# Performance work log

Measured on AMD Instinct MI355X. Metric: run time of the kernel, lower is better.

## Reference

```python
import jax, jax.numpy as jnp
import numpy as np

NUM_PPR_NODES = 262144
BATCH = 4096
K = NUM_PPR_NODES // BATCH  # ppr neighbors per batch node
F_IN, H, C = 256, 512, 64


def setup_inputs() -> dict:
    key = jax.random.key(0)
    ks = jax.random.split(key, 6)
    X = jax.random.normal(ks[0], (NUM_PPR_NODES, F_IN), dtype=jnp.float32)
    ppr_scores = jax.random.uniform(ks[1], (NUM_PPR_NODES,), dtype=jnp.float32)
    # sorted batch ids; last element == BATCH-1 so dim_size = ppr_idx[-1]+1 = BATCH
    ppr_idx = jnp.repeat(jnp.arange(BATCH, dtype=jnp.int64), K)
    s1 = 1.0 / np.sqrt(F_IN)
    s2 = 1.0 / np.sqrt(H)
    Wa = jax.random.uniform(ks[2], (F_IN, H), jnp.float32, -s1, s1)
    Wb = jax.random.uniform(ks[3], (H, H), jnp.float32, -s2, s2)
    Wc = jax.random.uniform(ks[4], (H, H), jnp.float32, -s2, s2)
    Wd = jax.random.uniform(ks[5], (H, C), jnp.float32, -s2, s2)
    return {"X": X, "ppr_scores": ppr_scores, "ppr_idx": ppr_idx,
            "Wa": Wa, "Wb": Wb, "Wc": Wc, "Wd": Wd}


def reference(X, ppr_scores, ppr_idx, Wa, Wb, Wc, Wd):
    # embedding MLP (dropout inactive at eval): Linear -> ReLU -> Linear, no bias
    emb = jax.nn.relu(X @ Wa) @ Wb                      # [N, H]
    # weighted scatter-sum over ppr neighborhoods
    weighted = emb * ppr_scores[:, None]                # [N, H]
    agg = jax.ops.segment_sum(weighted, ppr_idx, num_segments=BATCH)  # [B, H]
    # logit MLP: Linear -> ReLU -> Linear, no bias
    logits = jax.nn.relu(agg @ Wc) @ Wd                 # [B, C]
    return logits
```

## Files before the change

### kernel.cpp

```cpp
#include <hip/hip_runtime.h>

typedef short bs8 __attribute__((ext_vector_type(8)));
typedef float fx4 __attribute__((ext_vector_type(4)));

__device__ __forceinline__ unsigned short f2bf(float f) {
    unsigned u = __builtin_bit_cast(unsigned, f);
    u += 0x7FFFu + ((u >> 16) & 1u);
    return (unsigned short)(u >> 16);
}

__device__ __forceinline__ bs8 load_cvt8(const float* p) {
    fx4 u = *(const fx4*)p;
    fx4 v = *(const fx4*)(p + 4);
    bs8 r;
    r[0] = (short)f2bf(u[0]); r[1] = (short)f2bf(u[1]);
    r[2] = (short)f2bf(u[2]); r[3] = (short)f2bf(u[3]);
    r[4] = (short)f2bf(v[0]); r[5] = (short)f2bf(v[1]);
    r[6] = (short)f2bf(v[2]); r[7] = (short)f2bf(v[3]);
    return r;
}

__global__ void pack_b(const float* __restrict__ src, unsigned short* __restrict__ dst,
                       int KN, int N) {
    const int l = threadIdx.x;
    const int lr = l & 15, lg = l >> 4;
    const int bid = blockIdx.x;
    const int cf = bid / KN, kc = bid % KN;
    const int col  = cf * 16 + lr;
    const int krow = kc * 32 + lg * 8;
    const size_t ob = ((size_t)bid * 64 + l) * 8;
    #pragma unroll
    for (int j = 0; j < 8; ++j)
        dst[ob + j] = f2bf(src[(size_t)(krow + j) * N + col]);
}

__global__ __launch_bounds__(256) void wbc_gemm(const float* __restrict__ Wb,
                                                const float* __restrict__ Wc,
                                                float* __restrict__ Wbc) {
    __shared__ float As[32][33];
    __shared__ float Bs[32][33];
    const int tx = threadIdx.x & 15, ty = threadIdx.x >> 4;
    const int i0 = blockIdx.y * 32, j0 = blockIdx.x * 32;
    float c00 = 0.f, c01 = 0.f, c10 = 0.f, c11 = 0.f;
    for (int k0 = 0; k0 < 512; k0 += 32) {
        for (int t = threadIdx.x; t < 1024; t += 256) {
            int r = t >> 5, c = t & 31;
            As[r][c] = Wb[(size_t)(i0 + r) * 512 + k0 + c];
            Bs[r][c] = Wc[(size_t)(k0 + r) * 512 + j0 + c];
        }
        __syncthreads();
        #pragma unroll
        for (int k = 0; k < 32; ++k) {
            float a0 = As[ty * 2][k], a1 = As[ty * 2 + 1][k];
            float b0 = Bs[k][tx * 2], b1 = Bs[k][tx * 2 + 1];
            c00 += a0 * b0; c01 += a0 * b1; c10 += a1 * b0; c11 += a1 * b1;
        }
        __syncthreads();
    }
    Wbc[(size_t)(i0 + ty * 2) * 512 + j0 + tx * 2]         = c00;
    Wbc[(size_t)(i0 + ty * 2) * 512 + j0 + tx * 2 + 1]     = c01;
    Wbc[(size_t)(i0 + ty * 2 + 1) * 512 + j0 + tx * 2]     = c10;
    Wbc[(size_t)(i0 + ty * 2 + 1) * 512 + j0 + tx * 2 + 1] = c11;
}

__global__ __launch_bounds__(256, 2) void k1_fused(
    const float* __restrict__ X, const float* __restrict__ scores,
    const bs8* __restrict__ WaP, unsigned short* __restrict__ aggH) {
    __shared__ unsigned short xt[64 * 256];

    const int tid = threadIdx.x;
    const int seg = blockIdx.x;
    const size_t row0 = (size_t)seg * 64;

    #pragma unroll
    for (int it = 0; it < 8; ++it) {
        const int flat = it * 2048 + tid * 8;
        const int r = flat >> 8, c = flat & 255;
        bs8 v = load_cvt8(X + (row0 + r) * 256 + c);
        int byte = r * 512 + c * 2;
        byte ^= (r & 7) << 4;
        *(bs8*)((char*)xt + byte) = v;
    }
    __syncthreads();

    const int w = tid >> 6, l = tid & 63;
    const int lr = l & 15, lg = l >> 4;

    #pragma unroll 1
    for (int ci = 0; ci < 2; ++ci) {
        const int cc = w * 2 + ci;
        fx4 acc[4][4];
        #pragma unroll
        for (int mf = 0; mf < 4; ++mf)
            #pragma unroll
            for (int nf = 0; nf < 4; ++nf)
                acc[mf][nf] = (fx4){0.f, 0.f, 0.f, 0.f};

        #pragma unroll
        for (int kc = 0; kc < 8; ++kc) {
            bs8 b[4];
            #pragma unroll
            for (int nf = 0; nf < 4; ++nf)
                b[nf] = WaP[((cc * 4 + nf) * 8 + kc) * 64 + l];
            bs8 a[4];
            #pragma unroll
            for (int mf = 0; mf < 4; ++mf) {
                const int row = mf * 16 + lr;
                int byte = row * 512 + kc * 64 + lg * 16;
                byte ^= (row & 7) << 4;
                a[mf] = *(const bs8*)((const char*)xt + byte);
            }
            #pragma unroll
            for (int mf = 0; mf < 4; ++mf)
                #pragma unroll
                for (int nf = 0; nf < 4; ++nf)
                    acc[mf][nf] = __builtin_amdgcn_mfma_f32_16x16x32_bf16(
                        a[mf], b[nf], acc[mf][nf], 0, 0, 0);
        }

        float sc0[4][4];
        #pragma unroll
        for (int mf = 0; mf < 4; ++mf) {
            fx4 s = *(const fx4*)(scores + row0 + mf * 16 + lg * 4);
            sc0[mf][0] = s[0]; sc0[mf][1] = s[1]; sc0[mf][2] = s[2]; sc0[mf][3] = s[3];
        }
        #pragma unroll
        for (int nf = 0; nf < 4; ++nf) {
            float p = 0.f;
            #pragma unroll
            for (int mf = 0; mf < 4; ++mf)
                #pragma unroll
                for (int r = 0; r < 4; ++r) {
                    float v = acc[mf][nf][r];
                    v = v > 0.f ? v : 0.f;
                    p += v * sc0[mf][r];
                }
            p += __shfl_xor(p, 16, 64);
            p += __shfl_xor(p, 32, 64);
            if (lg == 0)
                aggH[(size_t)seg * 512 + cc * 64 + nf * 16 + lr] = f2bf(p);
        }
    }
}

__global__ __launch_bounds__(256) void k2_gemm(
    const unsigned short* __restrict__ aggH, const bs8* __restrict__ WbcP,
    unsigned short* __restrict__ T) {
    const int tid = threadIdx.x;
    const int w = tid >> 6, l = tid & 63, lr = l & 15, lg = l >> 4;
    const int gw = blockIdx.x * 4 + w;
    const int rg = gw >> 3, cg = gw & 7;
    const int r0 = rg * 64, c0 = cg * 64;

    fx4 acc[4][4];
    #pragma unroll
    for (int mf = 0; mf < 4; ++mf)
        #pragma unroll
        for (int nf = 0; nf < 4; ++nf)
            acc[mf][nf] = (fx4){0.f, 0.f, 0.f, 0.f};

    #pragma unroll 1
    for (int kc = 0; kc < 16; ++kc) {
        bs8 a[4], b[4];
        #pragma unroll
        for (int mf = 0; mf < 4; ++mf)
            a[mf] = *(const bs8*)(aggH + (size_t)(r0 + mf * 16 + lr) * 512 + kc * 32 + lg * 8);
        #pragma unroll
        for (int nf = 0; nf < 4; ++nf)
            b[nf] = WbcP[((cg * 4 + nf) * 16 + kc) * 64 + l];
        #pragma unroll
        for (int mf = 0; mf < 4; ++mf)
            #pragma unroll
            for (int nf = 0; nf < 4; ++nf)
                acc[mf][nf] = __builtin_amdgcn_mfma_f32_16x16x32_bf16(
                    a[mf], b[nf], acc[mf][nf], 0, 0, 0);
    }
    #pragma unroll
    for (int mf = 0; mf < 4; ++mf)
        #pragma unroll
        for (int nf = 0; nf < 4; ++nf)
            #pragma unroll
            for (int r = 0; r < 4; ++r) {
                float v = fmaxf(acc[mf][nf][r], 0.f);
                T[(size_t)(r0 + mf * 16 + lg * 4 + r) * 512 + c0 + nf * 16 + lr] = f2bf(v);
            }
}

__global__ __launch_bounds__(256) void k3_gemm(
    const unsigned short* __restrict__ T, const bs8* __restrict__ WdP,
    float* __restrict__ out) {
    const int tid = threadIdx.x;
    const int w = tid >> 6, l = tid & 63, lr = l & 15, lg = l >> 4;
    const int gw = blockIdx.x * 4 + w;
    const int r0 = gw * 64;

    fx4 acc[4][4];
    #pragma unroll
    for (int mf = 0; mf < 4; ++mf)
        #pragma unroll
        for (int nf = 0; nf < 4; ++nf)
            acc[mf][nf] = (fx4){0.f, 0.f, 0.f, 0.f};

    #pragma unroll 1
    for (int kc = 0; kc < 16; ++kc) {
        bs8 a[4], b[4];
        #pragma unroll
        for (int mf = 0; mf < 4; ++mf)
            a[mf] = *(const bs8*)(T + (size_t)(r0 + mf * 16 + lr) * 512 + kc * 32 + lg * 8);
        #pragma unroll
        for (int nf = 0; nf < 4; ++nf)
            b[nf] = WdP[(nf * 16 + kc) * 64 + l];
        #pragma unroll
        for (int mf = 0; mf < 4; ++mf)
            #pragma unroll
            for (int nf = 0; nf < 4; ++nf)
                acc[mf][nf] = __builtin_amdgcn_mfma_f32_16x16x32_bf16(
                    a[mf], b[nf], acc[mf][nf], 0, 0, 0);
    }
    #pragma unroll
    for (int mf = 0; mf < 4; ++mf)
        #pragma unroll
        for (int nf = 0; nf < 4; ++nf)
            #pragma unroll
            for (int r = 0; r < 4; ++r)
                out[(size_t)(r0 + mf * 16 + lg * 4 + r) * 64 + nf * 16 + lr] = acc[mf][nf][r];
}

extern "C" void kernel_launch(void* const* d_in, const int* in_sizes, int n_in,
                              void* d_out, int out_size, void* d_ws, size_t ws_size,
                              hipStream_t stream) {
    const float* X  = (const float*)d_in[0];
    const float* sc = (const float*)d_in[1];
    const float* Wa = (const float*)d_in[3];
    const float* Wb = (const float*)d_in[4];
    const float* Wc = (const float*)d_in[5];
    const float* Wd = (const float*)d_in[6];
    float* out = (float*)d_out;

    char* ws = (char*)d_ws;
    unsigned short* WaP  = (unsigned short*)(ws + 0);
    unsigned short* WbcP = (unsigned short*)(ws + 262144);
    unsigned short* WdP  = (unsigned short*)(ws + 786432);
    float*          Wbc  = (float*)         (ws + 851968);
    unsigned short* aggH = (unsigned short*)(ws + 1900544);
    unsigned short* T    = (unsigned short*)(ws + 6094848);

    pack_b<<<dim3(32 * 8),  dim3(64), 0, stream>>>(Wa,  WaP,  8,  512);
    wbc_gemm<<<dim3(16, 16), dim3(256), 0, stream>>>(Wb, Wc, Wbc);
    pack_b<<<dim3(32 * 16), dim3(64), 0, stream>>>(Wbc, WbcP, 16, 512);
    pack_b<<<dim3(4 * 16),  dim3(64), 0, stream>>>(Wd,  WdP,  16, 64);

    k1_fused<<<dim3(4096), dim3(256), 0, stream>>>(X, sc, (const bs8*)WaP, aggH);
    k2_gemm<<<dim3(128),   dim3(256), 0, stream>>>(aggH, (const bs8*)WbcP, T);
    k3_gemm<<<dim3(16),    dim3(256), 0, stream>>>(T, (const bs8*)WdP, out);
}
```

Before: 189.5 us.

## Make k1 persistent over 8 segments with async LDS prefetch and register-resident Wa

k1_fused now runs 512 blocks of 512 threads, each looping over 8 segments. Each of the 8 waves owns one 64-column slice of H, and its packed Wa fragments stay in registers across segments instead of being reloaded. The next segment's fp32 X rows are prefetched straight into an LDS staging strip with global_load_lds while the current segment's MFMA work runs, then converted to swizzled bf16 in a double buffer. The aim is to hide X load latency and drop the repeated Wa traffic, at the cost of heavy register and LDS use (64KB strip plus 64KB double buffer), fewer resident blocks, and extra barriers.

```diff
diff --git a/kernel.cpp b/kernel.cpp
--- a/kernel.cpp
+++ b/kernel.cpp
@@ -2,6 +2,8 @@
 
 typedef short bs8 __attribute__((ext_vector_type(8)));
 typedef float fx4 __attribute__((ext_vector_type(4)));
+typedef unsigned int u32;
+typedef unsigned long long u64;
 
 __device__ __forceinline__ unsigned short f2bf(float f) {
     unsigned u = __builtin_bit_cast(unsigned, f);
@@ -9,15 +11,10 @@
     return (unsigned short)(u >> 16);
 }
 
-__device__ __forceinline__ bs8 load_cvt8(const float* p) {
-    fx4 u = *(const fx4*)p;
-    fx4 v = *(const fx4*)(p + 4);
-    bs8 r;
-    r[0] = (short)f2bf(u[0]); r[1] = (short)f2bf(u[1]);
-    r[2] = (short)f2bf(u[2]); r[3] = (short)f2bf(u[3]);
-    r[4] = (short)f2bf(v[0]); r[5] = (short)f2bf(v[1]);
-    r[6] = (short)f2bf(v[2]); r[7] = (short)f2bf(v[3]);
-    return r;
+__device__ __forceinline__ void gld16(const void* g, void* l) {
+    __builtin_amdgcn_global_load_lds(
+        (const __attribute__((address_space(1))) void*)g,
+        (__attribute__((address_space(3))) void*)l, 16, 0, 0);
 }
 
 __global__ void pack_b(const float* __restrict__ src, unsigned short* __restrict__ dst,
@@ -63,32 +60,62 @@
     Wbc[(size_t)(i0 + ty * 2 + 1) * 512 + j0 + tx * 2 + 1] = c11;
 }
 
-__global__ __launch_bounds__(256, 2) void k1_fused(
+__global__ __launch_bounds__(512, 2) void k1_fused(
     const float* __restrict__ X, const float* __restrict__ scores,
     const bs8* __restrict__ WaP, unsigned short* __restrict__ aggH) {
-    __shared__ unsigned short xt[64 * 256];
+    __shared__ float strip[16384];
+    __shared__ unsigned short xt[2][16384];
 
     const int tid = threadIdx.x;
-    const int seg = blockIdx.x;
-    const size_t row0 = (size_t)seg * 64;
-
-    #pragma unroll
-    for (int it = 0; it < 8; ++it) {
-        const int flat = it * 2048 + tid * 8;
-        const int r = flat >> 8, c = flat & 255;
-        bs8 v = load_cvt8(X + (row0 + r) * 256 + c);
-        int byte = r * 512 + c * 2;
-        byte ^= (r & 7) << 4;
-        *(bs8*)((char*)xt + byte) = v;
-    }
-    __syncthreads();
-
     const int w = tid >> 6, l = tid & 63;
     const int lr = l & 15, lg = l >> 4;
 
+    bs8 bfr[4][8];
+    #pragma unroll
+    for (int nf = 0; nf < 4; ++nf)
+        #pragma unroll
+        for (int kc = 0; kc < 8; ++kc)
+            bfr[nf][kc] = WaP[(((w * 4 + nf) * 8) + kc) * 64 + l];
+
+    const int seg0 = blockIdx.x * 8;
+
+    {
+        const char* src = (const char*)(X + (size_t)seg0 * 16384) + w * 1024 + l * 16;
+        char* dst = (char*)strip + w * 1024;
+        #pragma unroll
+        for (int j = 0; j < 8; ++j)
+            gld16(src + j * 8192, dst + j * 8192);
+    }
+
     #pragma unroll 1
-    for (int ci = 0; ci < 2; ++ci) {
-        const int cc = w * 2 + ci;
+    for (int s = 0; s < 8; ++s) {
+        const int seg = seg0 + s;
+        unsigned short* buf = xt[s & 1];
+
+        asm volatile("s_waitcnt vmcnt(0)" ::: "memory");
+        __builtin_amdgcn_sched_barrier(0);
+
+        #pragma unroll
+        for (int j = 0; j < 8; ++j) {
+            fx4 v = *(const fx4*)((const char*)strip + tid * 16 + j * 8192);
+            const int row = j * 8 + w;
+            const int col = (tid & 63) * 4;
+            u32 p0 = (u32)f2bf(v[0]) | ((u32)f2bf(v[1]) << 16);
+            u32 p1 = (u32)f2bf(v[2]) | ((u32)f2bf(v[3]) << 16);
+            int byte = row * 512 + col * 2;
+            byte ^= (row & 7) << 4;
+            *(u64*)((char*)buf + byte) = (u64)p0 | ((u64)p1 << 32);
+        }
+        __syncthreads();
+
+        if (s + 1 < 8) {
+            const char* src = (const char*)(X + (size_t)(seg + 1) * 16384) + w * 1024 + l * 16;
+            char* dst = (char*)strip + w * 1024;
+            #pragma unroll
+            for (int j = 0; j < 8; ++j)
+                gld16(src + j * 8192, dst + j * 8192);
+        }
+
         fx4 acc[4][4];
         #pragma unroll
         for (int mf = 0; mf < 4; ++mf)
@@ -98,31 +125,28 @@
 
         #pragma unroll
         for (int kc = 0; kc < 8; ++kc) {
-            bs8 b[4];
-            #pragma unroll
-            for (int nf = 0; nf < 4; ++nf)
-                b[nf] = WaP[((cc * 4 + nf) * 8 + kc) * 64 + l];
             bs8 a[4];
             #pragma unroll
             for (int mf = 0; mf < 4; ++mf) {
                 const int row = mf * 16 + lr;
                 int byte = row * 512 + kc * 64 + lg * 16;
                 byte ^= (row & 7) << 4;
-                a[mf] = *(const bs8*)((const char*)xt + byte);
+                a[mf] = *(const bs8*)((const char*)buf + byte);
             }
             #pragma unroll
             for (int mf = 0; mf < 4; ++mf)
                 #pragma unroll
                 for (int nf = 0; nf < 4; ++nf)
                     acc[mf][nf] = __builtin_amdgcn_mfma_f32_16x16x32_bf16(
-                        a[mf], b[nf], acc[mf][nf], 0, 0, 0);
-        }
-
+                        a[mf], bfr[nf][kc], acc[mf][nf], 0, 0, 0);
+        }
+
+        const size_t row0 = (size_t)seg * 64;
         float sc0[4][4];
         #pragma unroll
         for (int mf = 0; mf < 4; ++mf) {
-            fx4 s = *(const fx4*)(scores + row0 + mf * 16 + lg * 4);
-            sc0[mf][0] = s[0]; sc0[mf][1] = s[1]; sc0[mf][2] = s[2]; sc0[mf][3] = s[3];
+            fx4 sv = *(const fx4*)(scores + row0 + mf * 16 + lg * 4);
+            sc0[mf][0] = sv[0]; sc0[mf][1] = sv[1]; sc0[mf][2] = sv[2]; sc0[mf][3] = sv[3];
         }
         #pragma unroll
         for (int nf = 0; nf < 4; ++nf) {
@@ -138,8 +162,9 @@
             p += __shfl_xor(p, 16, 64);
             p += __shfl_xor(p, 32, 64);
             if (lg == 0)
-                aggH[(size_t)seg * 512 + cc * 64 + nf * 16 + lr] = f2bf(p);
-        }
+                aggH[(size_t)seg * 512 + w * 64 + nf * 16 + lr] = f2bf(p);
+        }
+        __syncthreads();
     }
 }
 
@@ -250,7 +275,7 @@
     pack_b<<<dim3(32 * 16), dim3(64), 0, stream>>>(Wbc, WbcP, 16, 512);
     pack_b<<<dim3(4 * 16),  dim3(64), 0, stream>>>(Wd,  WdP,  16, 64);
 
-    k1_fused<<<dim3(4096), dim3(256), 0, stream>>>(X, sc, (const bs8*)WaP, aggH);
-    k2_gemm<<<dim3(128),   dim3(256), 0, stream>>>(aggH, (const bs8*)WbcP, T);
-    k3_gemm<<<dim3(16),    dim3(256), 0, stream>>>(T, (const bs8*)WdP, out);
-}
+    k1_fused<<<dim3(512), dim3(512), 0, stream>>>(X, sc, (const bs8*)WaP, aggH);
+    k2_gemm<<<dim3(128),  dim3(256), 0, stream>>>(aggH, (const bs8*)WbcP, T);
+    k3_gemm<<<dim3(16),   dim3(256), 0, stream>>>(T, (const bs8*)WdP, out);
+}
```

Measured after the change: 271.0 us. 1.43x slower.

## Split X bf16 conversion into separate pass and use direct global-to-LDS loads

Applied to the files above, without the earlier changes.

Converts X from fp32 to bf16 in a separate grid-stride kernel writing to workspace, then the GEMM kernel loads swizzled bf16 tiles straight into LDS via global_load_lds. Processing is chunked according to available workspace size, and the score loads are hoisted out of the column loop. The intent is to simplify the GEMM's load path and reduce per-block conversion latency, at the cost of an extra write and read of a bf16 copy of X through memory.

```diff
diff --git a/kernel.cpp b/kernel.cpp
--- a/kernel.cpp
+++ b/kernel.cpp
@@ -2,6 +2,7 @@
 
 typedef short bs8 __attribute__((ext_vector_type(8)));
 typedef float fx4 __attribute__((ext_vector_type(4)));
+typedef unsigned int u32;
 
 __device__ __forceinline__ unsigned short f2bf(float f) {
     unsigned u = __builtin_bit_cast(unsigned, f);
@@ -9,15 +10,10 @@
     return (unsigned short)(u >> 16);
 }
 
-__device__ __forceinline__ bs8 load_cvt8(const float* p) {
-    fx4 u = *(const fx4*)p;
-    fx4 v = *(const fx4*)(p + 4);
-    bs8 r;
-    r[0] = (short)f2bf(u[0]); r[1] = (short)f2bf(u[1]);
-    r[2] = (short)f2bf(u[2]); r[3] = (short)f2bf(u[3]);
-    r[4] = (short)f2bf(v[0]); r[5] = (short)f2bf(v[1]);
-    r[6] = (short)f2bf(v[2]); r[7] = (short)f2bf(v[3]);
-    return r;
+__device__ __forceinline__ void gld16(const void* g, void* l) {
+    __builtin_amdgcn_global_load_lds(
+        (const __attribute__((address_space(1))) void*)g,
+        (__attribute__((address_space(3))) void*)l, 16, 0, 0);
 }
 
 __global__ void pack_b(const float* __restrict__ src, unsigned short* __restrict__ dst,
@@ -63,28 +59,53 @@
     Wbc[(size_t)(i0 + ty * 2 + 1) * 512 + j0 + tx * 2 + 1] = c11;
 }
 
-__global__ __launch_bounds__(256, 2) void k1_fused(
-    const float* __restrict__ X, const float* __restrict__ scores,
-    const bs8* __restrict__ WaP, unsigned short* __restrict__ aggH) {
-    __shared__ unsigned short xt[64 * 256];
+__global__ __launch_bounds__(256) void cvt_bf16(const float* __restrict__ src,
+                                                unsigned short* __restrict__ dst,
+                                                long n8) {
+    const long stride = (long)gridDim.x * 256;
+    for (long i = (long)blockIdx.x * 256 + threadIdx.x; i < n8; i += stride) {
+        fx4 u = *(const fx4*)(src + i * 8);
+        fx4 v = *(const fx4*)(src + i * 8 + 4);
+        bs8 r;
+        r[0] = (short)f2bf(u[0]); r[1] = (short)f2bf(u[1]);
+        r[2] = (short)f2bf(u[2]); r[3] = (short)f2bf(u[3]);
+        r[4] = (short)f2bf(v[0]); r[5] = (short)f2bf(v[1]);
+        r[6] = (short)f2bf(v[2]); r[7] = (short)f2bf(v[3]);
+        *(bs8*)(dst + i * 8) = r;
+    }
+}
+
+__global__ __launch_bounds__(256) void k1_gemm(
+    const unsigned short* __restrict__ Xb,
+    const float* __restrict__ scores,
+    const bs8* __restrict__ WaP,
+    unsigned short* __restrict__ aggH,
+    int seg_base) {
+    __shared__ unsigned short xb[16384];
 
     const int tid = threadIdx.x;
-    const int seg = blockIdx.x;
-    const size_t row0 = (size_t)seg * 64;
-
-    #pragma unroll
-    for (int it = 0; it < 8; ++it) {
-        const int flat = it * 2048 + tid * 8;
-        const int r = flat >> 8, c = flat & 255;
-        bs8 v = load_cvt8(X + (row0 + r) * 256 + c);
-        int byte = r * 512 + c * 2;
-        byte ^= (r & 7) << 4;
-        *(bs8*)((char*)xt + byte) = v;
-    }
-    __syncthreads();
-
     const int w = tid >> 6, l = tid & 63;
     const int lr = l & 15, lg = l >> 4;
+    const int seg = seg_base + blockIdx.x;
+    const size_t tile0 = (size_t)blockIdx.x * 32768;
+
+    #pragma unroll
+    for (int j = 0; j < 8; ++j) {
+        const int d  = j * 4096 + w * 1024;
+        const int dl = d + l * 16;
+        const int s  = dl ^ (((dl >> 9) & 7) << 4);
+        gld16((const char*)Xb + tile0 + s, (char*)xb + d);
+    }
+    asm volatile("s_waitcnt vmcnt(0)" ::: "memory");
+    __syncthreads();
+
+    const size_t row0 = (size_t)seg * 64;
+    float sc0[4][4];
+    #pragma unroll
+    for (int mf = 0; mf < 4; ++mf) {
+        fx4 sv = *(const fx4*)(scores + row0 + mf * 16 + lg * 4);
+        sc0[mf][0] = sv[0]; sc0[mf][1] = sv[1]; sc0[mf][2] = sv[2]; sc0[mf][3] = sv[3];
+    }
 
     #pragma unroll 1
     for (int ci = 0; ci < 2; ++ci) {
@@ -106,9 +127,8 @@
             #pragma unroll
             for (int mf = 0; mf < 4; ++mf) {
                 const int row = mf * 16 + lr;
-                int byte = row * 512 + kc * 64 + lg * 16;
-                byte ^= (row & 7) << 4;
-                a[mf] = *(const bs8*)((const char*)xt + byte);
+                const int x = row * 512 + kc * 64 + lg * 16;
+                a[mf] = *(const bs8*)((const char*)xb + (x ^ ((row & 7) << 4)));
             }
             #pragma unroll
             for (int mf = 0; mf < 4; ++mf)
@@ -118,12 +138,6 @@
                         a[mf], b[nf], acc[mf][nf], 0, 0, 0);
         }
 
-        float sc0[4][4];
-        #pragma unroll
-        for (int mf = 0; mf < 4; ++mf) {
-            fx4 s = *(const fx4*)(scores + row0 + mf * 16 + lg * 4);
-            sc0[mf][0] = s[0]; sc0[mf][1] = s[1]; sc0[mf][2] = s[2]; sc0[mf][3] = s[3];
-        }
         #pragma unroll
         for (int nf = 0; nf < 4; ++nf) {
             float p = 0.f;
@@ -244,13 +258,32 @@
     float*          Wbc  = (float*)         (ws + 851968);
     unsigned short* aggH = (unsigned short*)(ws + 1900544);
     unsigned short* T    = (unsigned short*)(ws + 6094848);
+    const size_t xb_off  = 12582912;
+    unsigned short* Xb   = (unsigned short*)(ws + xb_off);
+    const size_t xb_full = (size_t)262144 * 256 * 2;
+
+    int chunk_segs;
+    if      (ws_size >= xb_off + xb_full)      chunk_segs = 4096;
+    else if (ws_size >= xb_off + xb_full / 4)  chunk_segs = 1024;
+    else if (ws_size >= xb_off + xb_full / 16) chunk_segs = 256;
+    else                                       chunk_segs = 64;
 
     pack_b<<<dim3(32 * 8),  dim3(64), 0, stream>>>(Wa,  WaP,  8,  512);
     wbc_gemm<<<dim3(16, 16), dim3(256), 0, stream>>>(Wb, Wc, Wbc);
     pack_b<<<dim3(32 * 16), dim3(64), 0, stream>>>(Wbc, WbcP, 16, 512);
     pack_b<<<dim3(4 * 16),  dim3(64), 0, stream>>>(Wd,  WdP,  16, 64);
 
-    k1_fused<<<dim3(4096), dim3(256), 0, stream>>>(X, sc, (const bs8*)WaP, aggH);
-    k2_gemm<<<dim3(128),   dim3(256), 0, stream>>>(aggH, (const bs8*)WbcP, T);
-    k3_gemm<<<dim3(16),    dim3(256), 0, stream>>>(T, (const bs8*)WdP, out);
-}
+    const int npairs = 4096 / chunk_segs;
+    for (int c = 0; c < npairs; ++c) {
+        const float* Xc = X + (size_t)c * chunk_segs * 16384;
+        const long n8 = (long)chunk_segs * 16384 / 8;
+        int blocks = (int)((n8 + 255) / 256);
+        if (blocks > 4096) blocks = 4096;
+        cvt_bf16<<<dim3(blocks), dim3(256), 0, stream>>>(Xc, Xb, n8);
+        k1_gemm<<<dim3(chunk_segs), dim3(256), 0, stream>>>(
+            Xb, sc, (const bs8*)WaP, aggH, c * chunk_segs);
+    }
+
+    k2_gemm<<<dim3(128), dim3(256), 0, stream>>>(aggH, (const bs8*)WbcP, T);
+    k3_gemm<<<dim3(16),  dim3(256), 0, stream>>>(T, (const bs8*)WdP, out);
+}
```

Result: slower. 275.1 us (+45.2%).

## Process two segments per block in k1 to reuse Wa fragments, prefetch B

Applied to the files above, without the earlier changes.

Each k1 block now loads and converts two 64-row segments of X into two LDS tiles, so every Wa fragment loaded from global memory feeds MFMAs for both segments. The Wa fragments for the next k-chunk are prefetched while the current one computes. X is read with nontemporal loads so it does not evict cached weights. A small warm kernel touches packed Wa beforehand to pull it into cache. This halves the grid and doubles shared memory and accumulator registers per block, which may lower occupancy.

```diff
diff --git a/kernel.cpp b/kernel.cpp
--- a/kernel.cpp
+++ b/kernel.cpp
@@ -9,9 +9,9 @@
     return (unsigned short)(u >> 16);
 }
 
-__device__ __forceinline__ bs8 load_cvt8(const float* p) {
-    fx4 u = *(const fx4*)p;
-    fx4 v = *(const fx4*)(p + 4);
+__device__ __forceinline__ bs8 load_cvt8_nt(const float* p) {
+    fx4 u = __builtin_nontemporal_load((const fx4*)p);
+    fx4 v = __builtin_nontemporal_load((const fx4*)(p + 4));
     bs8 r;
     r[0] = (short)f2bf(u[0]); r[1] = (short)f2bf(u[1]);
     r[2] = (short)f2bf(u[2]); r[3] = (short)f2bf(u[3]);
@@ -32,6 +32,11 @@
     #pragma unroll
     for (int j = 0; j < 8; ++j)
         dst[ob + j] = f2bf(src[(size_t)(krow + j) * N + col]);
+}
+
+__global__ __launch_bounds__(256) void warm(const float* __restrict__ p, float* __restrict__ sink) {
+    float s = p[blockIdx.x * 256 + threadIdx.x];
+    if (s == 1e30f) sink[0] = s;
 }
 
 __global__ __launch_bounds__(256) void wbc_gemm(const float* __restrict__ Wb,
@@ -66,20 +71,22 @@
 __global__ __launch_bounds__(256, 2) void k1_fused(
     const float* __restrict__ X, const float* __restrict__ scores,
     const bs8* __restrict__ WaP, unsigned short* __restrict__ aggH) {
-    __shared__ unsigned short xt[64 * 256];
+    __shared__ unsigned short xt[2][16384];
 
     const int tid = threadIdx.x;
-    const int seg = blockIdx.x;
-    const size_t row0 = (size_t)seg * 64;
-
-    #pragma unroll
-    for (int it = 0; it < 8; ++it) {
-        const int flat = it * 2048 + tid * 8;
-        const int r = flat >> 8, c = flat & 255;
-        bs8 v = load_cvt8(X + (row0 + r) * 256 + c);
-        int byte = r * 512 + c * 2;
-        byte ^= (r & 7) << 4;
-        *(bs8*)((char*)xt + byte) = v;
+    const size_t rowbase = (size_t)blockIdx.x * 128;
+
+    #pragma unroll
+    for (int t = 0; t < 2; ++t) {
+        #pragma unroll
+        for (int it = 0; it < 8; ++it) {
+            const int flat = it * 2048 + tid * 8;
+            const int r = flat >> 8, c = flat & 255;
+            bs8 v = load_cvt8_nt(X + (rowbase + t * 64 + r) * 256 + c);
+            int byte = r * 512 + c * 2;
+            byte ^= (r & 7) << 4;
+            *(bs8*)((char*)xt[t] + byte) = v;
+        }
     }
     __syncthreads();
 
@@ -88,57 +95,80 @@
 
     #pragma unroll 1
     for (int ci = 0; ci < 2; ++ci) {
-        const int cc = w * 2 + ci;
-        fx4 acc[4][4];
-        #pragma unroll
-        for (int mf = 0; mf < 4; ++mf)
-            #pragma unroll
-            for (int nf = 0; nf < 4; ++nf)
-                acc[mf][nf] = (fx4){0.f, 0.f, 0.f, 0.f};
-
-        #pragma unroll
+        const int cbase = w * 8 + ci * 4;
+        fx4 acc0[4][4], acc1[4][4];
+        #pragma unroll
+        for (int mf = 0; mf < 4; ++mf)
+            #pragma unroll
+            for (int j = 0; j < 4; ++j) {
+                acc0[mf][j] = (fx4){0.f, 0.f, 0.f, 0.f};
+                acc1[mf][j] = (fx4){0.f, 0.f, 0.f, 0.f};
+            }
+
+        bs8 b[4];
+        #pragma unroll
+        for (int j = 0; j < 4; ++j)
+            b[j] = WaP[(size_t)((cbase + j) * 8) * 64 + l];
+
+        #pragma unroll 1
         for (int kc = 0; kc < 8; ++kc) {
-            bs8 b[4];
-            #pragma unroll
-            for (int nf = 0; nf < 4; ++nf)
-                b[nf] = WaP[((cc * 4 + nf) * 8 + kc) * 64 + l];
-            bs8 a[4];
+            const int nk = (kc + 1) & 7;
+            bs8 nb[4];
+            #pragma unroll
+            for (int j = 0; j < 4; ++j)
+                nb[j] = WaP[(size_t)((cbase + j) * 8 + nk) * 64 + l];
+
+            bs8 a0[4], a1[4];
             #pragma unroll
             for (int mf = 0; mf < 4; ++mf) {
                 const int row = mf * 16 + lr;
-                int byte = row * 512 + kc * 64 + lg * 16;
-                byte ^= (row & 7) << 4;
-                a[mf] = *(const bs8*)((const char*)xt + byte);
+                const int x = row * 512 + kc * 64 + lg * 16;
+                const int sx = x ^ ((row & 7) << 4);
+                a0[mf] = *(const bs8*)((const char*)xt[0] + sx);
+                a1[mf] = *(const bs8*)((const char*)xt[1] + sx);
             }
             #pragma unroll
             for (int mf = 0; mf < 4; ++mf)
                 #pragma unroll
-                for (int nf = 0; nf < 4; ++nf)
-                    acc[mf][nf] = __builtin_amdgcn_mfma_f32_16x16x32_bf16(
-                        a[mf], b[nf], acc[mf][nf], 0, 0, 0);
-        }
-
-        float sc0[4][4];
-        #pragma unroll
-        for (int mf = 0; mf < 4; ++mf) {
-            fx4 s = *(const fx4*)(scores + row0 + mf * 16 + lg * 4);
-            sc0[mf][0] = s[0]; sc0[mf][1] = s[1]; sc0[mf][2] = s[2]; sc0[mf][3] = s[3];
-        }
-        #pragma unroll
-        for (int nf = 0; nf < 4; ++nf) {
-            float p = 0.f;
+                for (int j = 0; j < 4; ++j)
+                    acc0[mf][j] = __builtin_amdgcn_mfma_f32_16x16x32_bf16(
+                        a0[mf], b[j], acc0[mf][j], 0, 0, 0);
             #pragma unroll
             for (int mf = 0; mf < 4; ++mf)
                 #pragma unroll
-                for (int r = 0; r < 4; ++r) {
-                    float v = acc[mf][nf][r];
-                    v = v > 0.f ? v : 0.f;
-                    p += v * sc0[mf][r];
-                }
-            p += __shfl_xor(p, 16, 64);
-            p += __shfl_xor(p, 32, 64);
-            if (lg == 0)
-                aggH[(size_t)seg * 512 + cc * 64 + nf * 16 + lr] = f2bf(p);
+                for (int j = 0; j < 4; ++j)
+                    acc1[mf][j] = __builtin_amdgcn_mfma_f32_16x16x32_bf16(
+                        a1[mf], b[j], acc1[mf][j], 0, 0, 0);
+            #pragma unroll
+            for (int j = 0; j < 4; ++j) b[j] = nb[j];
+        }
+
+        #pragma unroll
+        for (int t = 0; t < 2; ++t) {
+            const size_t seg = (size_t)blockIdx.x * 2 + t;
+            float sct[4][4];
+            #pragma unroll
+            for (int mf = 0; mf < 4; ++mf) {
+                fx4 sv = *(const fx4*)(scores + seg * 64 + mf * 16 + lg * 4);
+                sct[mf][0] = sv[0]; sct[mf][1] = sv[1];
+                sct[mf][2] = sv[2]; sct[mf][3] = sv[3];
+            }
+            #pragma unroll
+            for (int j = 0; j < 4; ++j) {
+                float p = 0.f;
+                #pragma unroll
+                for (int mf = 0; mf < 4; ++mf)
+                    #pragma unroll
+                    for (int r = 0; r < 4; ++r) {
+                        float v = t == 0 ? acc0[mf][j][r] : acc1[mf][j][r];
+                        v = v > 0.f ? v : 0.f;
+                        p += v * sct[mf][r];
+                    }
+                p += __shfl_xor(p, 16, 64);
+                p += __shfl_xor(p, 32, 64);
+                if (lg == 0)
+                    aggH[seg * 512 + (cbase + j) * 16 + lr] = f2bf(p);
+            }
         }
     }
 }
@@ -244,13 +274,16 @@
     float*          Wbc  = (float*)         (ws + 851968);
     unsigned short* aggH = (unsigned short*)(ws + 1900544);
     unsigned short* T    = (unsigned short*)(ws + 6094848);
+    float*          sink = (float*)         (ws + 11534336);
 
     pack_b<<<dim3(32 * 8),  dim3(64), 0, stream>>>(Wa,  WaP,  8,  512);
     wbc_gemm<<<dim3(16, 16), dim3(256), 0, stream>>>(Wb, Wc, Wbc);
     pack_b<<<dim3(32 * 16), dim3(64), 0, stream>>>(Wbc, WbcP, 16, 512);
     pack_b<<<dim3(4 * 16),  dim3(64), 0, stream>>>(Wd,  WdP,  16, 64);
 
-    k1_fused<<<dim3(4096), dim3(256), 0, stream>>>(X, sc, (const bs8*)WaP, aggH);
+    warm<<<dim3(256), dim3(256), 0, stream>>>((const float*)WaP, sink);
+
+    k1_fused<<<dim3(2048), dim3(256), 0, stream>>>(X, sc, (const bs8*)WaP, aggH);
     k2_gemm<<<dim3(128),   dim3(256), 0, stream>>>(aggH, (const bs8*)WbcP, T);
     k3_gemm<<<dim3(16),    dim3(256), 0, stream>>>(T, (const bs8*)WdP, out);
 }
```

New measurement: 169.1 us. 1.12x faster.
